# Kernel tuning notes

Hardware: AMD Instinct MI355X
Metric: run time of the kernel (lower is better)

The kernel has to match this reference:

```python
import jax, jax.numpy as jnp
import numpy as np

TEMPERATURE = 1.0
D_THRESH = 0.1
EPS = 1e-10
NORM_EPS = 1e-12  # F.normalize clamp


def _l2_normalize(x):
    n = jnp.sqrt(jnp.sum(x * x, axis=1, keepdims=True))
    return x / jnp.maximum(n, NORM_EPS)


def setup_inputs() -> dict:
    key = jax.random.key(0)
    k1, k2, k3 = jax.random.split(key, 3)
    N, D = 8192, 128
    f1 = jax.random.normal(k1, (N, D), dtype=jnp.float32)
    f2 = jax.random.normal(k2, (N, D), dtype=jnp.float32)
    # continuous targets in [-1, 1) so both the distance mask (|ti-tj|>0.1)
    # and the polarity mask (sign mismatch) are exercised
    targets = jax.random.uniform(k3, (N,), dtype=jnp.float32, minval=-1.0, maxval=1.0)
    return {"f1": f1, "f2": f2, "targets": targets}


def reference(f1, f2, targets):
    f1 = _l2_normalize(f1)
    f2 = _l2_normalize(f2)

    # self_mask: 1 where pair is a negative (far target or opposite polarity)
    dist_t = jnp.abs(targets[:, None] - targets[None, :])  # [N,N]
    mask_distance = dist_t > D_THRESH
    polarity = targets > 0
    mask_polarity = polarity[:, None] != polarity[None, :]
    self_mask = (mask_distance | mask_polarity).astype(f1.dtype)  # [N,N]

    # ||f1_i - f2_j||^2 via the cdist/matmul trick (avoids [N,N,D] tensor)
    sq1 = jnp.sum(f1 * f1, axis=1)  # [N]
    sq2 = jnp.sum(f2 * f2, axis=1)  # [N]
    dist = sq1[:, None] - 2.0 * (f1 @ f2.T) + sq2[None, :]  # [N,N]
    cos = 1.0 - 0.5 * dist

    p = jax.nn.softmax(cos / TEMPERATURE, axis=1)  # [N,N]
    pos_w = 1.0 - self_mask
    log_pos = -jnp.log(p + EPS) * pos_w
    log_neg = -jnp.log(1.0 - p + EPS) * self_mask
    per_row = (jnp.sum(log_pos, axis=1) / jnp.sum(pos_w, axis=1)
               + jnp.sum(log_neg, axis=1) / jnp.sum(self_mask, axis=1))
    return jnp.mean(per_row)
```

## Files before the change

kernel.cpp:

```cpp
#include <hip/hip_runtime.h>
#include <hip/hip_bf16.h>
#include <math.h>

#define NROWS 8192
#define DDIM  128
#define JCHUNKS 16
#define JPER  (NROWS / JCHUNKS)
#define STAGE_COLS 64
#define NSTAGES (JPER / STAGE_COLS)
#define ROWS_PER_BLOCK 128
#define GRIDX (NROWS / ROWS_PER_BLOCK)
#define LOG2E 1.44269504088896f

#define AS1 __attribute__((address_space(1)))
#define AS3 __attribute__((address_space(3)))

typedef __attribute__((ext_vector_type(8))) short bf16x8;
typedef __attribute__((ext_vector_type(4))) float f32x4;
typedef __attribute__((ext_vector_type(2))) float f32x2;

__global__ __launch_bounds__(256) void norm_kernel(
    const float* __restrict__ f1, const float* __restrict__ f2,
    __hip_bfloat16* __restrict__ f1b, __hip_bfloat16* __restrict__ f2b,
    float* __restrict__ out) {
  if (blockIdx.x == 0 && threadIdx.x == 0) out[0] = 0.0f;
  int t = threadIdx.x;
  int rloc = t >> 5;
  int l = t & 31;
  int b = blockIdx.x;
  int half = (b >= NROWS / 8) ? 1 : 0;
  int row = (b - half * (NROWS / 8)) * 8 + rloc;
  const float* src = half ? f2 : f1;
  __hip_bfloat16* dst = half ? f2b : f1b;

  float4 v = ((const float4*)src)[row * (DDIM / 4) + l];
  float s = v.x * v.x + v.y * v.y + v.z * v.z + v.w * v.w;
  #pragma unroll
  for (int off = 1; off < 32; off <<= 1) s += __shfl_xor(s, off, 64);
  float inv = 1.0f / fmaxf(sqrtf(s), 1e-12f);
  __hip_bfloat16 hv[4];
  hv[0] = __float2bfloat16(v.x * inv);
  hv[1] = __float2bfloat16(v.y * inv);
  hv[2] = __float2bfloat16(v.z * inv);
  hv[3] = __float2bfloat16(v.w * inv);
  *(ushort4*)&dst[(size_t)row * DDIM + l * 4] = *(ushort4*)hv;
}

__global__ __launch_bounds__(256, 4) void stats_kernel(
    const __hip_bfloat16* __restrict__ f1b,
    const __hip_bfloat16* __restrict__ f2b,
    const float* __restrict__ targets,
    float* __restrict__ partials) {
  __shared__ __align__(16) char lds0[STAGE_COLS * 256];
  __shared__ __align__(16) char lds1[STAGE_COLS * 256];
  __shared__ __align__(16) float tsh[JPER];

  const int chunk = blockIdx.y;
  const int i0 = blockIdx.x * ROWS_PER_BLOCK;
  const int w    = threadIdx.x >> 6;
  const int lane = threadIdx.x & 63;
  const int p15  = lane & 15;
  const int rl4  = lane >> 4;
  const int rbase = i0 + w * 32;

  bf16x8 afrag[2][4];
  #pragma unroll
  for (int rs = 0; rs < 2; ++rs) {
    const __hip_bfloat16* arow =
        &f1b[(size_t)(rbase + rs * 16 + p15) * DDIM + rl4 * 8];
    #pragma unroll
    for (int ks = 0; ks < 4; ++ks)
      afrag[rs][ks] = *(const bf16x8*)(arow + ks * 32);
  }

  f32x2 ti2[4];
  #pragma unroll
  for (int rr = 0; rr < 4; ++rr) {
    ti2[rr][0] = targets[rbase + rl4 * 4 + rr];
    ti2[rr][1] = targets[rbase + 16 + rl4 * 4 + rr];
  }

  f32x2 Z2[4]  = {{0,0},{0,0},{0,0},{0,0}};
  f32x2 Zp2[4] = {{0,0},{0,0},{0,0},{0,0}};
  f32x2 Cp2[4] = {{0,0},{0,0},{0,0},{0,0}};
  f32x2 Np2[4] = {{0,0},{0,0},{0,0},{0,0}};

  const int jb0 = chunk * JPER;

  int srcoff[4];
  #pragma unroll
  for (int q = 0; q < 4; ++q) {
    int rloc = w * 16 + q * 4 + rl4;
    int c    = p15 ^ (q * 4 + rl4);
    srcoff[q] = rloc * DDIM + c * 8;
  }

  {
    #pragma unroll
    for (int rnd = 0; rnd < 2; ++rnd)
      __builtin_amdgcn_global_load_lds(
          (const AS1 void*)(targets + jb0 + rnd * 256 + w * 64 + lane),
          (AS3 void*)(&tsh[rnd * 256 + w * 64]), 4, 0, 0);
    const __hip_bfloat16* gstage = f2b + (size_t)jb0 * DDIM;
    char* lbase = &lds0[w * 4096];
    #pragma unroll
    for (int q = 0; q < 4; ++q)
      __builtin_amdgcn_global_load_lds((const AS1 void*)(gstage + srcoff[q]),
                                       (AS3 void*)(lbase + q * 1024), 16, 0, 0);
  }

  for (int s = 0; s < NSTAGES; ++s) {
    __syncthreads();

    if (s + 1 < NSTAGES) {
      const __hip_bfloat16* gstage = f2b + (size_t)(jb0 + (s + 1) * STAGE_COLS) * DDIM;
      char* lbase = ((s + 1) & 1) ? &lds1[w * 4096] : &lds0[w * 4096];
      #pragma unroll
      for (int q = 0; q < 4; ++q)
        __builtin_amdgcn_global_load_lds((const AS1 void*)(gstage + srcoff[q]),
                                         (AS3 void*)(lbase + q * 1024), 16, 0, 0);
    }

    const char* lb = (s & 1) ? lds1 : lds0;
    #pragma unroll
    for (int ct = 0; ct < 4; ++ct) {
      const int rloc = ct * 16 + p15;
      bf16x8 bfrag[4];
      #pragma unroll
      for (int ks = 0; ks < 4; ++ks)
        bfrag[ks] = *(const bf16x8*)(lb + rloc * 256 + (((rl4 + ks * 4) ^ p15) << 4));

      float tj = tsh[s * STAGE_COLS + ct * 16 + p15];

      f32x4 acc0 = {0.f, 0.f, 0.f, 0.f};
      f32x4 acc1 = {0.f, 0.f, 0.f, 0.f};
      #pragma unroll
      for (int ks = 0; ks < 4; ++ks) {
        acc0 = __builtin_amdgcn_mfma_f32_16x16x32_bf16(afrag[0][ks], bfrag[ks], acc0, 0, 0, 0);
        acc1 = __builtin_amdgcn_mfma_f32_16x16x32_bf16(afrag[1][ks], bfrag[ks], acc1, 0, 0, 0);
      }

      const bool pj = tj > 0.0f;
      const f32x2 tjs = {tj, tj};
      const f32x2 Ks = {LOG2E, LOG2E};
      #pragma unroll
      for (int rr = 0; rr < 4; ++rr) {
        f32x2 c2 = {acc0[rr], acc1[rr]};
        f32x2 d2 = ti2[rr] - tjs;
        bool q0 = (__builtin_fabsf(d2[0]) <= 0.1f) & ((ti2[rr][0] > 0.0f) == pj);
        bool q1 = (__builtin_fabsf(d2[1]) <= 0.1f) & ((ti2[rr][1] > 0.0f) == pj);
        f32x2 m2 = {q0 ? 1.0f : 0.0f, q1 ? 1.0f : 0.0f};
        f32x2 x2 = c2 * Ks - Ks;
        f32x2 e2 = {__builtin_amdgcn_exp2f(x2[0]), __builtin_amdgcn_exp2f(x2[1])};
        Z2[rr]  += e2;
        Zp2[rr] += m2 * e2;
        Cp2[rr] += m2 * c2;
        Np2[rr] += m2;
      }
    }
  }

  #pragma unroll
  for (int rr = 0; rr < 4; ++rr) {
    for (int off = 1; off < 16; off <<= 1) {
      Z2[rr][0]  += __shfl_xor(Z2[rr][0],  off, 64);
      Z2[rr][1]  += __shfl_xor(Z2[rr][1],  off, 64);
      Zp2[rr][0] += __shfl_xor(Zp2[rr][0], off, 64);
      Zp2[rr][1] += __shfl_xor(Zp2[rr][1], off, 64);
      Cp2[rr][0] += __shfl_xor(Cp2[rr][0], off, 64);
      Cp2[rr][1] += __shfl_xor(Cp2[rr][1], off, 64);
      Np2[rr][0] += __shfl_xor(Np2[rr][0], off, 64);
      Np2[rr][1] += __shfl_xor(Np2[rr][1], off, 64);
    }
  }
  if (p15 == 0) {
    #pragma unroll
    for (int rs = 0; rs < 2; ++rs)
      #pragma unroll
      for (int rr = 0; rr < 4; ++rr) {
        size_t row = rbase + rs * 16 + rl4 * 4 + rr;
        f32x4 st = {Z2[rr][rs], Zp2[rr][rs], Cp2[rr][rs], Np2[rr][rs]};
        *(f32x4*)&partials[((size_t)row * JCHUNKS + chunk) * 4] = st;
      }
  }
}

__global__ void finalize_rows(const float* __restrict__ partials,
                              float* __restrict__ out) {
  int r = blockIdx.x * 256 + threadIdx.x;
  float Z = 0, Zp = 0, Cp = 0, Np = 0;
  for (int ch = 0; ch < JCHUNKS; ++ch) {
    float4 p = *(const float4*)&partials[((size_t)r * JCHUNKS + ch) * 4];
    Z += p.x; Zp += p.y; Cp += p.z; Np += p.w;
  }
  float Zn = Z - Zp;
  float nn = (float)NROWS - Np;
  float spos = (1.0f + logf(Z)) - Cp / Np;
  float sneg = Zn / Z - nn * 1e-10f;
  float per_row = spos + sneg / nn;

  float v = per_row;
  for (int off = 32; off; off >>= 1) v += __shfl_xor(v, off, 64);
  __shared__ float wsum[4];
  int lane = threadIdx.x & 63, wid = threadIdx.x >> 6;
  if (lane == 0) wsum[wid] = v;
  __syncthreads();
  if (threadIdx.x == 0)
    atomicAdd(out, (wsum[0] + wsum[1] + wsum[2] + wsum[3]) * (1.0f / (float)NROWS));
}

extern "C" void kernel_launch(void* const* d_in, const int* in_sizes, int n_in,
                              void* d_out, int out_size, void* d_ws, size_t ws_size,
                              hipStream_t stream) {
  const float* f1  = (const float*)d_in[0];
  const float* f2  = (const float*)d_in[1];
  const float* tgt = (const float*)d_in[2];
  float* out = (float*)d_out;

  char* ws = (char*)d_ws;
  __hip_bfloat16* f1b = (__hip_bfloat16*)ws;
  __hip_bfloat16* f2b = (__hip_bfloat16*)(ws + (size_t)NROWS * DDIM * 2);
  float* partials = (float*)(ws + (size_t)NROWS * DDIM * 4);

  norm_kernel<<<2 * (NROWS / 8), 256, 0, stream>>>(f1, f2, f1b, f2b, out);
  dim3 g2(GRIDX, JCHUNKS);
  stats_kernel<<<g2, 256, 0, stream>>>(f1b, f2b, tgt, partials);
  finalize_rows<<<NROWS / 256, 256, 0, stream>>>(partials, out);
}
```

Baseline: 101.1 us.

## Use 2 waves per block with 64 rows each to halve LDS B-fragment reads

The stats kernel now runs with 128 threads (2 waves) per block, and each wave covers 64 rows with four A-fragment sets instead of 32 rows with two. Each B fragment read from LDS now feeds four MFMA row tiles, which halves LDS reads per MFMA. Each wave also issues twice as many global-to-LDS stage loads. The cost is higher register pressure (four accumulator sets plus A fragments) and fewer waves per CU, which may reduce latency hiding.

```diff
diff --git a/kernel.cpp b/kernel.cpp
--- a/kernel.cpp
+++ b/kernel.cpp
@@ -17,7 +17,6 @@
 
 typedef __attribute__((ext_vector_type(8))) short bf16x8;
 typedef __attribute__((ext_vector_type(4))) float f32x4;
-typedef __attribute__((ext_vector_type(2))) float f32x2;
 
 __global__ __launch_bounds__(256) void norm_kernel(
     const float* __restrict__ f1, const float* __restrict__ f2,
@@ -46,7 +45,7 @@
   *(ushort4*)&dst[(size_t)row * DDIM + l * 4] = *(ushort4*)hv;
 }
 
-__global__ __launch_bounds__(256, 4) void stats_kernel(
+__global__ __launch_bounds__(128, 2) void stats_kernel(
     const __hip_bfloat16* __restrict__ f1b,
     const __hip_bfloat16* __restrict__ f2b,
     const float* __restrict__ targets,
@@ -61,11 +60,11 @@
   const int lane = threadIdx.x & 63;
   const int p15  = lane & 15;
   const int rl4  = lane >> 4;
-  const int rbase = i0 + w * 32;
-
-  bf16x8 afrag[2][4];
-  #pragma unroll
-  for (int rs = 0; rs < 2; ++rs) {
+  const int rbase = i0 + w * 64;
+
+  bf16x8 afrag[4][4];
+  #pragma unroll
+  for (int rs = 0; rs < 4; ++rs) {
     const __hip_bfloat16* arow =
         &f1b[(size_t)(rbase + rs * 16 + p15) * DDIM + rl4 * 8];
     #pragma unroll
@@ -73,38 +72,42 @@
       afrag[rs][ks] = *(const bf16x8*)(arow + ks * 32);
   }
 
-  f32x2 ti2[4];
-  #pragma unroll
-  for (int rr = 0; rr < 4; ++rr) {
-    ti2[rr][0] = targets[rbase + rl4 * 4 + rr];
-    ti2[rr][1] = targets[rbase + 16 + rl4 * 4 + rr];
-  }
-
-  f32x2 Z2[4]  = {{0,0},{0,0},{0,0},{0,0}};
-  f32x2 Zp2[4] = {{0,0},{0,0},{0,0},{0,0}};
-  f32x2 Cp2[4] = {{0,0},{0,0},{0,0},{0,0}};
-  f32x2 Np2[4] = {{0,0},{0,0},{0,0},{0,0}};
+  f32x4 ki[4];
+  #pragma unroll
+  for (int rs = 0; rs < 4; ++rs)
+    #pragma unroll
+    for (int rr = 0; rr < 4; ++rr)
+      ki[rs][rr] = targets[rbase + rs * 16 + rl4 * 4 + rr];
+
+  f32x4 Z[4], Zp[4], Cp[4], Np[4];
+  #pragma unroll
+  for (int rs = 0; rs < 4; ++rs) {
+    Z[rs] = (f32x4){0.f, 0.f, 0.f, 0.f};
+    Zp[rs] = (f32x4){0.f, 0.f, 0.f, 0.f};
+    Cp[rs] = (f32x4){0.f, 0.f, 0.f, 0.f};
+    Np[rs] = (f32x4){0.f, 0.f, 0.f, 0.f};
+  }
 
   const int jb0 = chunk * JPER;
 
-  int srcoff[4];
-  #pragma unroll
-  for (int q = 0; q < 4; ++q) {
-    int rloc = w * 16 + q * 4 + rl4;
-    int c    = p15 ^ (q * 4 + rl4);
+  int srcoff[8];
+  #pragma unroll
+  for (int q = 0; q < 8; ++q) {
+    int rloc = w * 32 + q * 4 + rl4;
+    int c    = p15 ^ ((q * 4 + rl4) & 15);
     srcoff[q] = rloc * DDIM + c * 8;
   }
 
   {
     #pragma unroll
-    for (int rnd = 0; rnd < 2; ++rnd)
+    for (int rnd = 0; rnd < 4; ++rnd)
       __builtin_amdgcn_global_load_lds(
-          (const AS1 void*)(targets + jb0 + rnd * 256 + w * 64 + lane),
-          (AS3 void*)(&tsh[rnd * 256 + w * 64]), 4, 0, 0);
+          (const AS1 void*)(targets + jb0 + rnd * 128 + threadIdx.x),
+          (AS3 void*)(&tsh[rnd * 128 + w * 64]), 4, 0, 0);
     const __hip_bfloat16* gstage = f2b + (size_t)jb0 * DDIM;
-    char* lbase = &lds0[w * 4096];
-    #pragma unroll
-    for (int q = 0; q < 4; ++q)
+    char* lbase = &lds0[w * 8192];
+    #pragma unroll
+    for (int q = 0; q < 8; ++q)
       __builtin_amdgcn_global_load_lds((const AS1 void*)(gstage + srcoff[q]),
                                        (AS3 void*)(lbase + q * 1024), 16, 0, 0);
   }
@@ -114,9 +117,9 @@
 
     if (s + 1 < NSTAGES) {
       const __hip_bfloat16* gstage = f2b + (size_t)(jb0 + (s + 1) * STAGE_COLS) * DDIM;
-      char* lbase = ((s + 1) & 1) ? &lds1[w * 4096] : &lds0[w * 4096];
-      #pragma unroll
-      for (int q = 0; q < 4; ++q)
+      char* lbase = ((s + 1) & 1) ? &lds1[w * 8192] : &lds0[w * 8192];
+      #pragma unroll
+      for (int q = 0; q < 8; ++q)
         __builtin_amdgcn_global_load_lds((const AS1 void*)(gstage + srcoff[q]),
                                          (AS3 void*)(lbase + q * 1024), 16, 0, 0);
     }
@@ -131,55 +134,57 @@
         bfrag[ks] = *(const bf16x8*)(lb + rloc * 256 + (((rl4 + ks * 4) ^ p15) << 4));
 
       float tj = tsh[s * STAGE_COLS + ct * 16 + p15];
-
-      f32x4 acc0 = {0.f, 0.f, 0.f, 0.f};
-      f32x4 acc1 = {0.f, 0.f, 0.f, 0.f};
-      #pragma unroll
-      for (int ks = 0; ks < 4; ++ks) {
-        acc0 = __builtin_amdgcn_mfma_f32_16x16x32_bf16(afrag[0][ks], bfrag[ks], acc0, 0, 0, 0);
-        acc1 = __builtin_amdgcn_mfma_f32_16x16x32_bf16(afrag[1][ks], bfrag[ks], acc1, 0, 0, 0);
-      }
-
       const bool pj = tj > 0.0f;
-      const f32x2 tjs = {tj, tj};
-      const f32x2 Ks = {LOG2E, LOG2E};
-      #pragma unroll
-      for (int rr = 0; rr < 4; ++rr) {
-        f32x2 c2 = {acc0[rr], acc1[rr]};
-        f32x2 d2 = ti2[rr] - tjs;
-        bool q0 = (__builtin_fabsf(d2[0]) <= 0.1f) & ((ti2[rr][0] > 0.0f) == pj);
-        bool q1 = (__builtin_fabsf(d2[1]) <= 0.1f) & ((ti2[rr][1] > 0.0f) == pj);
-        f32x2 m2 = {q0 ? 1.0f : 0.0f, q1 ? 1.0f : 0.0f};
-        f32x2 x2 = c2 * Ks - Ks;
-        f32x2 e2 = {__builtin_amdgcn_exp2f(x2[0]), __builtin_amdgcn_exp2f(x2[1])};
-        Z2[rr]  += e2;
-        Zp2[rr] += m2 * e2;
-        Cp2[rr] += m2 * c2;
-        Np2[rr] += m2;
+      const f32x4 tj4 = {tj, tj, tj, tj};
+      const f32x4 K4  = {LOG2E, LOG2E, LOG2E, LOG2E};
+
+      #pragma unroll
+      for (int rs = 0; rs < 4; ++rs) {
+        f32x4 acc = {0.f, 0.f, 0.f, 0.f};
+        #pragma unroll
+        for (int ks = 0; ks < 4; ++ks)
+          acc = __builtin_amdgcn_mfma_f32_16x16x32_bf16(afrag[rs][ks], bfrag[ks], acc, 0, 0, 0);
+
+        f32x4 c4 = acc;
+        f32x4 d4 = ki[rs] - tj4;
+        f32x4 m4;
+        #pragma unroll
+        for (int rr = 0; rr < 4; ++rr) {
+          bool q = (__builtin_fabsf(d4[rr]) <= 0.1f) & ((ki[rs][rr] > 0.0f) == pj);
+          m4[rr] = q ? 1.0f : 0.0f;
+        }
+        f32x4 x4 = c4 * K4 - K4;
+        f32x4 e4;
+        #pragma unroll
+        for (int rr = 0; rr < 4; ++rr) e4[rr] = __builtin_amdgcn_exp2f(x4[rr]);
+        Z[rs]  += e4;
+        Zp[rs] += m4 * e4;
+        Cp[rs] += m4 * c4;
+        Np[rs] += m4;
       }
     }
   }
 
   #pragma unroll
-  for (int rr = 0; rr < 4; ++rr) {
-    for (int off = 1; off < 16; off <<= 1) {
-      Z2[rr][0]  += __shfl_xor(Z2[rr][0],  off, 64);
-      Z2[rr][1]  += __shfl_xor(Z2[rr][1],  off, 64);
-      Zp2[rr][0] += __shfl_xor(Zp2[rr][0], off, 64);
-      Zp2[rr][1] += __shfl_xor(Zp2[rr][1], off, 64);
-      Cp2[rr][0] += __shfl_xor(Cp2[rr][0], off, 64);
-      Cp2[rr][1] += __shfl_xor(Cp2[rr][1], off, 64);
-      Np2[rr][0] += __shfl_xor(Np2[rr][0], off, 64);
-      Np2[rr][1] += __shfl_xor(Np2[rr][1], off, 64);
+  for (int rs = 0; rs < 4; ++rs) {
+    #pragma unroll
+    for (int rr = 0; rr < 4; ++rr) {
+      #pragma unroll
+      for (int off = 1; off < 16; off <<= 1) {
+        Z[rs][rr]  += __shfl_xor(Z[rs][rr],  off, 64);
+        Zp[rs][rr] += __shfl_xor(Zp[rs][rr], off, 64);
+        Cp[rs][rr] += __shfl_xor(Cp[rs][rr], off, 64);
+        Np[rs][rr] += __shfl_xor(Np[rs][rr], off, 64);
+      }
     }
   }
   if (p15 == 0) {
     #pragma unroll
-    for (int rs = 0; rs < 2; ++rs)
+    for (int rs = 0; rs < 4; ++rs)
       #pragma unroll
       for (int rr = 0; rr < 4; ++rr) {
         size_t row = rbase + rs * 16 + rl4 * 4 + rr;
-        f32x4 st = {Z2[rr][rs], Zp2[rr][rs], Cp2[rr][rs], Np2[rr][rs]};
+        f32x4 st = {Z[rs][rr], Zp[rs][rr], Cp[rs][rr], Np[rs][rr]};
         *(f32x4*)&partials[((size_t)row * JCHUNKS + chunk) * 4] = st;
       }
   }
@@ -224,6 +229,6 @@
 
   norm_kernel<<<2 * (NROWS / 8), 256, 0, stream>>>(f1, f2, f1b, f2b, out);
   dim3 g2(GRIDX, JCHUNKS);
-  stats_kernel<<<g2, 256, 0, stream>>>(f1b, f2b, tgt, partials);
+  stats_kernel<<<g2, 128, 0, stream>>>(f1b, f2b, tgt, partials);
   finalize_rows<<<NROWS / 256, 256, 0, stream>>>(partials, out);
 }
```

Result: no change. 102.3 us (+1.3%).
